# Kernel optimization log

Hardware: AMD Instinct MI355X
Metric: run time of the kernel (lower is better)

The kernel has to match this reference:

```python
import jax, jax.numpy as jnp
import numpy as np

B, S, DIM = 2, 2048, 1024
EXPERT_DIM = 256
N_S, N_R, TOP_K = 2, 32, 4
EPS = 1e-6


def setup_inputs() -> dict:
    key = jax.random.key(0)
    ks = jax.random.split(key, 12)
    s1 = 1.0 / np.sqrt(DIM)        # fan-in init scale for Linear(dim, expert_dim)
    s2 = 1.0 / np.sqrt(EXPERT_DIM)  # fan-in init scale for Linear(expert_dim, dim)
    return {
        "x": jax.random.normal(ks[0], (B, S, DIM), jnp.float32),
        "rms_w": jnp.ones((DIM,), jnp.float32),
        "centroids": jax.random.normal(ks[1], (N_R, DIM), jnp.float32),
        # shared experts, stacked along leading expert axis
        "sW1": jax.random.normal(ks[2], (N_S, DIM, EXPERT_DIM), jnp.float32) * s1,
        "sb1": jax.random.normal(ks[3], (N_S, EXPERT_DIM), jnp.float32) * s1,
        "sW2": jax.random.normal(ks[4], (N_S, EXPERT_DIM, DIM), jnp.float32) * s2,
        "sb2": jax.random.normal(ks[5], (N_S, DIM), jnp.float32) * s2,
        # routed experts
        "rW1": jax.random.normal(ks[6], (N_R, DIM, EXPERT_DIM), jnp.float32) * s1,
        "rb1": jax.random.normal(ks[7], (N_R, EXPERT_DIM), jnp.float32) * s1,
        "rW2": jax.random.normal(ks[8], (N_R, EXPERT_DIM, DIM), jnp.float32) * s2,
        "rb2": jax.random.normal(ks[9], (N_R, DIM), jnp.float32) * s2,
    }


def _rmsnorm(x, w):
    xf = x.astype(jnp.float32)
    n = xf * jax.lax.rsqrt(jnp.mean(xf * xf, axis=-1, keepdims=True) + EPS)
    return w * n.astype(x.dtype)


def _experts(xf, W1, b1, W2, b2):
    # xf: [T, D]; W1: [E, D, H]; returns [E, T, D]
    # Expert = Sequential(Linear, Linear, GELU) -> gelu applied AFTER second linear
    h = jnp.einsum('td,edh->eth', xf, W1) + b1[:, None, :]
    o = jnp.einsum('eth,ehd->etd', h, W2) + b2[:, None, :]
    return jax.nn.gelu(o, approximate=False)


def reference(x, rms_w, centroids, sW1, sb1, sW2, sb2, rW1, rb1, rW2, rb2):
    xn = _rmsnorm(x, rms_w)                      # [B, S, D]
    xf = xn.reshape(-1, DIM)                     # [T, D]
    T = xf.shape[0]

    # shared experts: summed dense output
    shared = _experts(xf, sW1, sb1, sW2, sb2).sum(axis=0)   # [T, D]

    # routing
    affinity = jax.nn.softmax(xf @ centroids.T, axis=-1)    # [T, E]
    topk_scores, topk_idx = jax.lax.top_k(affinity, TOP_K)
    mask = jnp.zeros_like(affinity).at[jnp.arange(T)[:, None], topk_idx].set(topk_scores)

    # dense-compute-then-mask, faithful to original module
    routed_all = _experts(xf, rW1, rb1, rW2, rb2)           # [E, T, D]
    routed = jnp.einsum('te,etd->td', mask, routed_all)     # [T, D]

    y = xn + (shared + routed).reshape(B, S, DIM)
    return y, affinity
```

## Files before the change

kernel.cpp:

```cpp
#include <hip/hip_runtime.h>
#include <hip/hip_bf16.h>
#include <math.h>

#define T_TOK 4096
#define DIM   1024
#define HDIM  256
#define N_SH  2
#define N_RT  32
#define N_E   34
#define TOPK  4
#define TB    128
#define MAXPB 200
#define NSLOT 6
#define OSW   34

typedef short bf16x8 __attribute__((ext_vector_type(8)));
typedef float f32x4  __attribute__((ext_vector_type(4)));
typedef unsigned short u16x8 __attribute__((ext_vector_type(8)));

__device__ __forceinline__ ushort f2b(float v) {
    __hip_bfloat16 h = __float2bfloat16(v);
    return *reinterpret_cast<const ushort*>(&h);
}
__device__ __forceinline__ float b2f(ushort u) {
    unsigned int x = ((unsigned int)u) << 16;
    return __uint_as_float(x);
}
__device__ __forceinline__ float gelu_tanh(float x) {
    float z = 0.7978845608028654f * (x + 0.044715f * x * x * x);
    float e = __expf(2.0f * z);
    float t = 1.0f - 2.0f / (e + 1.0f);
    return 0.5f * x * (1.0f + t);
}

__device__ __forceinline__ void gload_lds16(const ushort* g, ushort* l) {
    __builtin_amdgcn_global_load_lds(
        (const __attribute__((address_space(1))) void*)g,
        (__attribute__((address_space(3))) void*)l,
        16, 0, 0);
}

template<int K, int N>
__global__ __launch_bounds__(256) void pack_weights(
    const float* __restrict__ srcS, const float* __restrict__ srcR,
    ushort* __restrict__ dst)
{
    const int e = blockIdx.y;
    const float* src = (e < N_SH) ? (srcS + (size_t)e * K * N)
                                  : (srcR + (size_t)(e - N_SH) * K * N);
    const int kt  = K / 32;
    const int k32 = blockIdx.x % kt;
    const int nc  = blockIdx.x / kt;
    const int tid = threadIdx.x;

    __shared__ ushort ls[32][137];

    #pragma unroll
    for (int it = 0; it < 4; ++it) {
        const int row = it * 8 + (tid >> 5);
        const int c4  = tid & 31;
        const float4 v = *(const float4*)(src + (size_t)(k32 * 32 + row) * N
                                          + nc * 128 + c4 * 4);
        ls[row][c4 * 4 + 0] = f2b(v.x);
        ls[row][c4 * 4 + 1] = f2b(v.y);
        ls[row][c4 * 4 + 2] = f2b(v.z);
        ls[row][c4 * 4 + 3] = f2b(v.w);
    }
    __syncthreads();

    #pragma unroll
    for (int it = 0; it < 2; ++it) {
        const int t8   = tid >> 5;
        const int lane = it * 32 + (tid & 31);
        const int l16 = lane & 15, lk = lane >> 4;
        u16x8 o;
        #pragma unroll
        for (int j = 0; j < 8; ++j)
            o[j] = ls[lk * 8 + j][t8 * 16 + l16];
        const size_t tile = (size_t)(nc * 8 + t8) * kt + k32;
        *(u16x8*)(dst + (size_t)e * K * N + tile * 512 + lane * 8) = o;
    }
}

__global__ __launch_bounds__(256) void rms_router_kernel(
    const float* __restrict__ x, const float* __restrict__ rms_w,
    const float* __restrict__ cent,
    ushort* __restrict__ xnb, float* __restrict__ aff_out,
    int* __restrict__ tk_e, float* __restrict__ sscore)
{
    const int t0  = blockIdx.x * 4;
    const int tid = threadIdx.x;
    const int wid = tid >> 6;
    const int lane = tid & 63;
    const int t = t0 + wid;

    __shared__ float xsh[4][DIM];
    __shared__ float logits[4][N_RT];

    float4 xv[4], wv[4];
    float ss = 0.f;
    #pragma unroll
    for (int q = 0; q < 4; ++q) {
        xv[q] = ((const float4*)(x + (size_t)t * DIM))[lane + 64 * q];
        ss += xv[q].x*xv[q].x + xv[q].y*xv[q].y + xv[q].z*xv[q].z + xv[q].w*xv[q].w;
    }
    #pragma unroll
    for (int o = 32; o > 0; o >>= 1) ss += __shfl_down(ss, o);
    const float rstd = rsqrtf(__shfl(ss, 0) * (1.0f / (float)DIM) + 1e-6f);

    #pragma unroll
    for (int q = 0; q < 4; ++q)
        wv[q] = ((const float4*)rms_w)[lane + 64 * q];

    #pragma unroll
    for (int q = 0; q < 4; ++q) {
        float4 nv;
        nv.x = xv[q].x * rstd * wv[q].x;
        nv.y = xv[q].y * rstd * wv[q].y;
        nv.z = xv[q].z * rstd * wv[q].z;
        nv.w = xv[q].w * rstd * wv[q].w;
        ushort4 xb = make_ushort4(f2b(nv.x), f2b(nv.y), f2b(nv.z), f2b(nv.w));
        ((ushort4*)(xnb + (size_t)t * DIM))[lane + 64 * q] = xb;
        ((float4*)xsh[wid])[lane + 64 * q] = nv;
    }
    __syncthreads();

    #pragma unroll
    for (int ei = 0; ei < 8; ++ei) {
        const int e = wid * 8 + ei;
        const float4* c4 = (const float4*)(cent + (size_t)e * DIM);
        float a0 = 0.f, a1 = 0.f, a2 = 0.f, a3 = 0.f;
        #pragma unroll
        for (int q = 0; q < 4; ++q) {
            const float4 cv = c4[lane + 64 * q];
            const float4 x0 = ((const float4*)xsh[0])[lane + 64 * q];
            const float4 x1 = ((const float4*)xsh[1])[lane + 64 * q];
            const float4 x2 = ((const float4*)xsh[2])[lane + 64 * q];
            const float4 x3 = ((const float4*)xsh[3])[lane + 64 * q];
            a0 += cv.x*x0.x + cv.y*x0.y + cv.z*x0.z + cv.w*x0.w;
            a1 += cv.x*x1.x + cv.y*x1.y + cv.z*x1.z + cv.w*x1.w;
            a2 += cv.x*x2.x + cv.y*x2.y + cv.z*x2.z + cv.w*x2.w;
            a3 += cv.x*x3.x + cv.y*x3.y + cv.z*x3.z + cv.w*x3.w;
        }
        #pragma unroll
        for (int o = 32; o > 0; o >>= 1) {
            a0 += __shfl_down(a0, o);
            a1 += __shfl_down(a1, o);
            a2 += __shfl_down(a2, o);
            a3 += __shfl_down(a3, o);
        }
        if (lane == 0) {
            logits[0][e] = a0; logits[1][e] = a1;
            logits[2][e] = a2; logits[3][e] = a3;
        }
    }
    __syncthreads();

    {
        float v = (lane < N_RT) ? logits[wid][lane] : -INFINITY;
        float m = v;
        #pragma unroll
        for (int o = 32; o > 0; o >>= 1) m = fmaxf(m, __shfl_xor(m, o));
        float p = (lane < N_RT) ? expf(v - m) : 0.f;
        float s = p;
        #pragma unroll
        for (int o = 32; o > 0; o >>= 1) s += __shfl_xor(s, o);
        const float a = p / s;
        if (lane < N_RT) aff_out[(size_t)t * N_RT + lane] = a;
        if (lane < N_SH) sscore[(size_t)t * NSLOT + lane] = 1.f;

        float vv = (lane < N_RT) ? a : -1.f;
        #pragma unroll
        for (int it = 0; it < TOPK; ++it) {
            float mx = vv;
            #pragma unroll
            for (int o = 32; o > 0; o >>= 1) mx = fmaxf(mx, __shfl_xor(mx, o));
            unsigned long long msk = __ballot(vv == mx);
            int sel = __ffsll((long long)msk) - 1;
            sel = (sel < 0) ? 0 : (sel & (N_RT - 1));
            if (lane == 0) {
                tk_e[(size_t)t * TOPK + it] = sel;
                sscore[(size_t)t * NSLOT + 2 + it] = mx;
            }
            if (lane == sel) vv = -1.f;
        }
    }
}

__global__ __launch_bounds__(64) void scatter_kernel(
    const int* __restrict__ tk_e, int* __restrict__ counts, int* __restrict__ lists)
{
    const int e    = blockIdx.x;
    const int lane = threadIdx.x;
    const unsigned long long lt = (1ull << lane) - 1ull;
    int base = 0;
    int* lst = lists + (size_t)e * T_TOK;
    for (int c = 0; c < T_TOK * TOPK; c += 256) {
        const int4 v = *(const int4*)(tk_e + c + lane * 4);
        const bool p0 = (v.x == e), p1 = (v.y == e), p2 = (v.z == e), p3 = (v.w == e);
        const unsigned long long m0 = __ballot(p0);
        const unsigned long long m1 = __ballot(p1);
        const unsigned long long m2 = __ballot(p2);
        const unsigned long long m3 = __ballot(p3);
        const int c0 = __popcll(m0), c1 = __popcll(m1), c2 = __popcll(m2);
        if (p0) lst[base + __popcll(m0 & lt)] = c + lane * 4 + 0;
        if (p1) lst[base + c0 + __popcll(m1 & lt)] = c + lane * 4 + 1;
        if (p2) lst[base + c0 + c1 + __popcll(m2 & lt)] = c + lane * 4 + 2;
        if (p3) lst[base + c0 + c1 + c2 + __popcll(m3 & lt)] = c + lane * 4 + 3;
        base += c0 + c1 + c2 + __popcll(m3);
    }
    if (lane == 0) counts[e] = base;
}

__global__ __launch_bounds__(256) void residual_init(
    const ushort* __restrict__ xnb, float* __restrict__ y)
{
    const int idx = blockIdx.x * 256 + threadIdx.x;
    const ushort4 xr = *(const ushort4*)(xnb + (size_t)idx * 4);
    float4 a;
    a.x = b2f(xr.x); a.y = b2f(xr.y); a.z = b2f(xr.z); a.w = b2f(xr.w);
    ((float4*)y)[idx] = a;
}

template<bool ATOMIC>
__global__ __launch_bounds__(512, 2) void moe_mfma(
    const ushort* __restrict__ xnb,
    const ushort* __restrict__ W1p, const ushort* __restrict__ W2p,
    const float* __restrict__ sb1, const float* __restrict__ sb2,
    const float* __restrict__ rb1, const float* __restrict__ rb2,
    const int* __restrict__ counts, const int* __restrict__ lists,
    const float* __restrict__ sscore,
    ushort* __restrict__ sbuf, float* __restrict__ y)
{
    const int bi  = blockIdx.x;
    const int tid = threadIdx.x;

    __shared__ int    toks[TB];
    __shared__ int    orow[TB];
    __shared__ float  tscs[TB];
    __shared__ ushort hlds[TB * HDIM];
    __shared__ ushort astage[2 * 4096];
    __shared__ ushort ostage[8 * 64 * OSW];

    int e_full;
    const float *b1, *b2;

    if (bi < 64) {
        e_full = bi >> 5;
        const int tile = bi & 31;
        if (tid < TB) {
            const int t = tile * TB + tid;
            toks[tid] = t;
            orow[tid] = ATOMIC ? t : t * NSLOT + e_full;
            tscs[tid] = 1.f;
        }
        b1 = sb1 + e_full * HDIM;  b2 = sb2 + e_full * DIM;
    } else {
        const int j = bi - 64;
        const int b = j & 7, pos = j >> 3;
        int e = -1, tile = 0, accum = 0;
        #pragma unroll
        for (int g = 0; g < 4; ++g) {
            const int eg = b + 8 * g;
            const int tg = (counts[eg] + TB - 1) / TB;
            if (e < 0 && pos < accum + tg) { e = eg; tile = pos - accum; }
            accum += tg;
        }
        if (e < 0) return;
        e_full = N_SH + e;
        const int cnt = counts[e];
        if (tid < TB) {
            const int idx = tile * TB + tid;
            if (idx < cnt) {
                const int lv = lists[(size_t)e * T_TOK + idx];
                const int t = (lv >> 2) & (T_TOK - 1);
                toks[tid] = t;
                orow[tid] = ATOMIC ? t : t * NSLOT + 2 + (lv & 3);
                tscs[tid] = ATOMIC ? sscore[(size_t)t * NSLOT + 2 + (lv & 3)] : 0.f;
            } else {
                toks[tid] = 0;
                orow[tid] = ATOMIC ? 0 : T_TOK * NSLOT;
                tscs[tid] = 0.f;
            }
        }
        b1 = rb1 + e * HDIM;  b2 = rb2 + e * DIM;
    }
    __syncthreads();

    const int w = tid >> 6, lane = tid & 63;
    const int l16 = lane & 15, lk = lane >> 4;
    const int mh = w >> 2;
    const int nq = w & 3;

    const ushort* W1e = W1p + (size_t)e_full * DIM * HDIM;
    const ushort* W2e = W2p + (size_t)e_full * HDIM * DIM;

    {
        const ushort* asrc = xnb + (size_t)toks[w * 16 + (lane >> 2)] * DIM
                             + (lane & 3) * 8;
        gload_lds16(asrc, astage + w * 512);

        const ushort* bbase[4];
        #pragma unroll
        for (int ni = 0; ni < 4; ++ni)
            bbase[ni] = W1e + (size_t)((nq * 4 + ni) * 32) * 512 + lane * 8;

        f32x4 acc[4][4];
        #pragma unroll
        for (int mi = 0; mi < 4; ++mi)
            #pragma unroll
            for (int ni = 0; ni < 4; ++ni) acc[mi][ni] = (f32x4){0.f,0.f,0.f,0.f};

        bf16x8 bc[4];
        #pragma unroll
        for (int ni = 0; ni < 4; ++ni) bc[ni] = *(const bf16x8*)bbase[ni];
        __syncthreads();

        #pragma unroll 2
        for (int k32 = 0; k32 < 32; ++k32) {
            const int cur = k32 & 1;
            bf16x8 bn[4];
            if (k32 < 31) {
                gload_lds16(asrc + (k32 + 1) * 32,
                            astage + (cur ^ 1) * 4096 + w * 512);
                #pragma unroll
                for (int ni = 0; ni < 4; ++ni)
                    bn[ni] = *(const bf16x8*)(bbase[ni] + (size_t)(k32 + 1) * 512);
            }
            bf16x8 a[4];
            #pragma unroll
            for (int mi = 0; mi < 4; ++mi) {
                const int tloc = mh * 64 + mi * 16 + l16;
                a[mi] = *(const bf16x8*)(astage + cur * 4096 + tloc * 32 + lk * 8);
            }
            #pragma unroll
            for (int ni = 0; ni < 4; ++ni)
                #pragma unroll
                for (int mi = 0; mi < 4; ++mi)
                    acc[mi][ni] = __builtin_amdgcn_mfma_f32_16x16x32_bf16(a[mi], bc[ni], acc[mi][ni], 0, 0, 0);
            if (k32 < 31) {
                #pragma unroll
                for (int ni = 0; ni < 4; ++ni) bc[ni] = bn[ni];
            }
            __syncthreads();
        }

        #pragma unroll
        for (int ni = 0; ni < 4; ++ni) {
            const int n = nq * 64 + ni * 16 + l16;
            const float bv = b1[n];
            #pragma unroll
            for (int mi = 0; mi < 4; ++mi) {
                #pragma unroll
                for (int r = 0; r < 4; ++r) {
                    const int m = mh * 64 + mi * 16 + lk * 4 + r;
                    const int byte = (m * (HDIM * 2) + n * 2) ^ ((m & 7) << 4);
                    *(ushort*)((char*)hlds + byte) = f2b(acc[mi][ni][r] + bv);
                }
            }
        }
    }
    __syncthreads();

    {
        for (int jc = 0; jc < 4; ++jc) {
            f32x4 acc2[4][4];
            #pragma unroll
            for (int mi = 0; mi < 4; ++mi)
                #pragma unroll
                for (int ni = 0; ni < 4; ++ni) acc2[mi][ni] = (f32x4){0.f,0.f,0.f,0.f};

            const ushort* b2base[4];
            #pragma unroll
            for (int ni = 0; ni < 4; ++ni)
                b2base[ni] = W2e + (size_t)((jc * 16 + nq * 4 + ni) * 8) * 512 + lane * 8;

            bf16x8 bc2[4];
            #pragma unroll
            for (int ni = 0; ni < 4; ++ni) bc2[ni] = *(const bf16x8*)b2base[ni];

            #pragma unroll
            for (int k32 = 0; k32 < 8; ++k32) {
                bf16x8 a2[4];
                #pragma unroll
                for (int mi = 0; mi < 4; ++mi) {
                    const int m = mh * 64 + mi * 16 + l16;
                    const int byte = (m * (HDIM * 2) + (k32 * 32 + lk * 8) * 2) ^ ((m & 7) << 4);
                    a2[mi] = *(const bf16x8*)((const char*)hlds + byte);
                }
                bf16x8 bn2[4];
                if (k32 < 7) {
                    #pragma unroll
                    for (int ni = 0; ni < 4; ++ni)
                        bn2[ni] = *(const bf16x8*)(b2base[ni] + (size_t)(k32 + 1) * 512);
                }
                #pragma unroll
                for (int ni = 0; ni < 4; ++ni)
                    #pragma unroll
                    for (int mi = 0; mi < 4; ++mi)
                        acc2[mi][ni] = __builtin_amdgcn_mfma_f32_16x16x32_bf16(a2[mi], bc2[ni], acc2[mi][ni], 0, 0, 0);
                if (k32 < 7) {
                    #pragma unroll
                    for (int ni = 0; ni < 4; ++ni) bc2[ni] = bn2[ni];
                }
            }

            if (ATOMIC) {
                #pragma unroll
                for (int ni = 0; ni < 4; ++ni) {
                    const int n = jc * 256 + nq * 64 + ni * 16 + l16;
                    const float bv = b2[n];
                    #pragma unroll
                    for (int mi = 0; mi < 4; ++mi)
                        #pragma unroll
                        for (int r = 0; r < 4; ++r) {
                            const int m = mi * 16 + lk * 4 + r;
                            const float val = gelu_tanh(acc2[mi][ni][r] + bv) * tscs[mh * 64 + m];
                            atomicAdd(&y[(size_t)orow[mh * 64 + m] * DIM + n], val);
                        }
                }
            } else {
                ushort* os = ostage + w * (64 * OSW);
                #pragma unroll
                for (int p = 0; p < 2; ++p) {
                    asm volatile("s_waitcnt lgkmcnt(0)" ::: "memory");
                    #pragma unroll
                    for (int q = 0; q < 2; ++q) {
                        const int ni = p * 2 + q;
                        const float bv = b2[jc * 256 + nq * 64 + ni * 16 + l16];
                        #pragma unroll
                        for (int mi = 0; mi < 4; ++mi)
                            #pragma unroll
                            for (int r = 0; r < 4; ++r) {
                                const int m = mi * 16 + lk * 4 + r;
                                os[m * OSW + q * 16 + l16] = f2b(acc2[mi][ni][r] + bv);
                            }
                    }
                    asm volatile("s_waitcnt lgkmcnt(0)" ::: "memory");
                    #pragma unroll
                    for (int rr = 0; rr < 4; ++rr) {
                        const int m  = rr * 16 + (lane >> 2);
                        const int nl = (lane & 3) * 8;
                        u16x8 vv = *(const u16x8*)(os + m * OSW + nl);
                        *(u16x8*)(sbuf + (size_t)orow[mh * 64 + m] * DIM
                                  + jc * 256 + nq * 64 + p * 32 + nl) = vv;
                    }
                }
            }
        }
    }
}

__global__ __launch_bounds__(256) void gather_kernel(
    const ushort* __restrict__ sbuf, const float* __restrict__ sscore,
    const ushort* __restrict__ xnb, float* __restrict__ y)
{
    const int idx = blockIdx.x * 256 + threadIdx.x;
    const int t = idx >> 8;
    const int d = (idx & 255) * 4;
    const ushort4 xr = *(const ushort4*)(xnb + (size_t)t * DIM + d);
    float4 a;
    a.x = b2f(xr.x); a.y = b2f(xr.y); a.z = b2f(xr.z); a.w = b2f(xr.w);
    #pragma unroll
    for (int s = 0; s < NSLOT; ++s) {
        const float sc = sscore[(size_t)t * NSLOT + s];
        const ushort4 u = *(const ushort4*)(sbuf + ((size_t)t * NSLOT + s) * DIM + d);
        a.x += gelu_tanh(b2f(u.x)) * sc;
        a.y += gelu_tanh(b2f(u.y)) * sc;
        a.z += gelu_tanh(b2f(u.z)) * sc;
        a.w += gelu_tanh(b2f(u.w)) * sc;
    }
    ((float4*)y)[idx] = a;
}

extern "C" void kernel_launch(void* const* d_in, const int* in_sizes, int n_in,
                              void* d_out, int out_size, void* d_ws, size_t ws_size,
                              hipStream_t stream) {
    const float* x      = (const float*)d_in[0];
    const float* rms_w  = (const float*)d_in[1];
    const float* cent   = (const float*)d_in[2];
    const float* sW1    = (const float*)d_in[3];
    const float* sb1    = (const float*)d_in[4];
    const float* sW2    = (const float*)d_in[5];
    const float* sb2    = (const float*)d_in[6];
    const float* rW1    = (const float*)d_in[7];
    const float* rb1    = (const float*)d_in[8];
    const float* rW2    = (const float*)d_in[9];
    const float* rb2    = (const float*)d_in[10];

    float* y_out   = (float*)d_out;
    float* aff_out = (float*)d_out + (size_t)T_TOK * DIM;

    char* p = (char*)d_ws;
    size_t off = 0;
    auto take = [&](size_t b) {
        char* r = p + off;
        off += (b + 255) & ~(size_t)255;
        return r;
    };
    ushort* xnb    = (ushort*)take((size_t)T_TOK * DIM * 2);
    ushort* W1p    = (ushort*)take((size_t)N_E * DIM * HDIM * 2);
    ushort* W2p    = (ushort*)take((size_t)N_E * HDIM * DIM * 2);
    int*    counts = (int*)take(N_RT * sizeof(int));
    int*    lists  = (int*)take((size_t)N_RT * T_TOK * 4);
    float*  sscore = (float*)take((size_t)T_TOK * NSLOT * 4);
    int*    tk_e   = (int*)take((size_t)T_TOK * TOPK * 4);
    ushort* sbuf   = (ushort*)take(((size_t)T_TOK * NSLOT + TB) * DIM * 2);
    const bool slot_ok = (off <= ws_size);

    pack_weights<DIM, HDIM><<<dim3(64, N_E), dim3(256), 0, stream>>>(sW1, rW1, W1p);
    pack_weights<HDIM, DIM><<<dim3(64, N_E), dim3(256), 0, stream>>>(sW2, rW2, W2p);

    rms_router_kernel<<<dim3(T_TOK / 4), dim3(256), 0, stream>>>(
        x, rms_w, cent, xnb, aff_out, tk_e, sscore);

    scatter_kernel<<<dim3(N_RT), dim3(64), 0, stream>>>(tk_e, counts, lists);

    const int grid = 64 + 8 * MAXPB;
    if (slot_ok) {
        moe_mfma<false><<<dim3(grid), dim3(512), 0, stream>>>(
            xnb, W1p, W2p, sb1, sb2, rb1, rb2, counts, lists,
            sscore, sbuf, y_out);
        gather_kernel<<<dim3((T_TOK * DIM / 4) / 256), dim3(256), 0, stream>>>(
            sbuf, sscore, xnb, y_out);
    } else {
        residual_init<<<dim3((T_TOK * DIM / 4) / 256), dim3(256), 0, stream>>>(
            xnb, y_out);
        moe_mfma<true><<<dim3(grid), dim3(512), 0, stream>>>(
            xnb, W1p, W2p, sb1, sb2, rb1, rb2, counts, lists,
            sscore, sbuf, y_out);
    }
}
```

Measured before the change: 142.8 us.

## Stage expert weight tiles through LDS, shared across wave halves

Both expert GEMMs now load W1/W2 k-slices cooperatively into a double-buffered LDS buffer (bstage) with async global-to-LDS copies. Previously each wave loaded its B fragments straight from global into registers, so the two M-halves of waves fetched identical weight data twice. The second GEMM's nested jc/k loops are flattened into a single 32-step pipelined loop with a barrier per step. This halves weight traffic and frees registers, at the cost of 32KB more LDS, extra LDS reads and more __syncthreads.

```diff
diff --git a/kernel.cpp b/kernel.cpp
--- a/kernel.cpp
+++ b/kernel.cpp
@@ -240,6 +240,7 @@
     __shared__ float  tscs[TB];
     __shared__ ushort hlds[TB * HDIM];
     __shared__ ushort astage[2 * 4096];
+    __shared__ ushort bstage[2 * 8192];
     __shared__ ushort ostage[8 * 64 * OSW];
 
     int e_full;
@@ -299,35 +300,34 @@
         const ushort* asrc = xnb + (size_t)toks[w * 16 + (lane >> 2)] * DIM
                              + (lane & 3) * 8;
         gload_lds16(asrc, astage + w * 512);
-
-        const ushort* bbase[4];
-        #pragma unroll
-        for (int ni = 0; ni < 4; ++ni)
-            bbase[ni] = W1e + (size_t)((nq * 4 + ni) * 32) * 512 + lane * 8;
+        #pragma unroll
+        for (int s2 = 0; s2 < 2; ++s2) {
+            const int q = w * 2 + s2;
+            gload_lds16(W1e + (size_t)(q * 32 + 0) * 512 + lane * 8,
+                        bstage + q * 512);
+        }
 
         f32x4 acc[4][4];
         #pragma unroll
         for (int mi = 0; mi < 4; ++mi)
             #pragma unroll
             for (int ni = 0; ni < 4; ++ni) acc[mi][ni] = (f32x4){0.f,0.f,0.f,0.f};
-
-        bf16x8 bc[4];
-        #pragma unroll
-        for (int ni = 0; ni < 4; ++ni) bc[ni] = *(const bf16x8*)bbase[ni];
         __syncthreads();
 
         #pragma unroll 2
         for (int k32 = 0; k32 < 32; ++k32) {
             const int cur = k32 & 1;
-            bf16x8 bn[4];
             if (k32 < 31) {
                 gload_lds16(asrc + (k32 + 1) * 32,
                             astage + (cur ^ 1) * 4096 + w * 512);
                 #pragma unroll
-                for (int ni = 0; ni < 4; ++ni)
-                    bn[ni] = *(const bf16x8*)(bbase[ni] + (size_t)(k32 + 1) * 512);
-            }
-            bf16x8 a[4];
+                for (int s2 = 0; s2 < 2; ++s2) {
+                    const int q = w * 2 + s2;
+                    gload_lds16(W1e + (size_t)(q * 32 + k32 + 1) * 512 + lane * 8,
+                                bstage + (cur ^ 1) * 8192 + q * 512);
+                }
+            }
+            bf16x8 a[4], bf[4];
             #pragma unroll
             for (int mi = 0; mi < 4; ++mi) {
                 const int tloc = mh * 64 + mi * 16 + l16;
@@ -335,14 +335,20 @@
             }
             #pragma unroll
             for (int ni = 0; ni < 4; ++ni)
+                bf[ni] = *(const bf16x8*)(bstage + cur * 8192 + (nq * 4 + ni) * 512 + lane * 8);
+            #pragma unroll
+            for (int ni = 0; ni < 4; ++ni)
                 #pragma unroll
                 for (int mi = 0; mi < 4; ++mi)
-                    acc[mi][ni] = __builtin_amdgcn_mfma_f32_16x16x32_bf16(a[mi], bc[ni], acc[mi][ni], 0, 0, 0);
-            if (k32 < 31) {
-                #pragma unroll
-                for (int ni = 0; ni < 4; ++ni) bc[ni] = bn[ni];
-            }
+                    acc[mi][ni] = __builtin_amdgcn_mfma_f32_16x16x32_bf16(a[mi], bf[ni], acc[mi][ni], 0, 0, 0);
             __syncthreads();
+        }
+
+        #pragma unroll
+        for (int s2 = 0; s2 < 2; ++s2) {
+            const int q = w * 2 + s2;
+            gload_lds16(W2e + (size_t)((0 * 16 + q) * 8 + 0) * 512 + lane * 8,
+                        bstage + q * 512);
         }
 
         #pragma unroll
@@ -363,90 +369,95 @@
     __syncthreads();
 
     {
-        for (int jc = 0; jc < 4; ++jc) {
-            f32x4 acc2[4][4];
-            #pragma unroll
-            for (int mi = 0; mi < 4; ++mi)
+        f32x4 acc2[4][4];
+        #pragma unroll
+        for (int mi = 0; mi < 4; ++mi)
+            #pragma unroll
+            for (int ni = 0; ni < 4; ++ni) acc2[mi][ni] = (f32x4){0.f,0.f,0.f,0.f};
+
+        #pragma unroll 2
+        for (int s = 0; s < 32; ++s) {
+            const int jc  = s >> 3;
+            const int k32 = s & 7;
+            const int cur = s & 1;
+
+            if (s < 31) {
+                const int s2 = s + 1;
+                const int jc2 = s2 >> 3, kk2 = s2 & 7;
                 #pragma unroll
-                for (int ni = 0; ni < 4; ++ni) acc2[mi][ni] = (f32x4){0.f,0.f,0.f,0.f};
-
-            const ushort* b2base[4];
+                for (int q2 = 0; q2 < 2; ++q2) {
+                    const int q = w * 2 + q2;
+                    gload_lds16(W2e + (size_t)((jc2 * 16 + q) * 8 + kk2) * 512 + lane * 8,
+                                bstage + (cur ^ 1) * 8192 + q * 512);
+                }
+            }
+
+            bf16x8 a2[4], bf2[4];
+            #pragma unroll
+            for (int mi = 0; mi < 4; ++mi) {
+                const int m = mh * 64 + mi * 16 + l16;
+                const int byte = (m * (HDIM * 2) + (k32 * 32 + lk * 8) * 2) ^ ((m & 7) << 4);
+                a2[mi] = *(const bf16x8*)((const char*)hlds + byte);
+            }
             #pragma unroll
             for (int ni = 0; ni < 4; ++ni)
-                b2base[ni] = W2e + (size_t)((jc * 16 + nq * 4 + ni) * 8) * 512 + lane * 8;
-
-            bf16x8 bc2[4];
-            #pragma unroll
-            for (int ni = 0; ni < 4; ++ni) bc2[ni] = *(const bf16x8*)b2base[ni];
-
-            #pragma unroll
-            for (int k32 = 0; k32 < 8; ++k32) {
-                bf16x8 a2[4];
+                bf2[ni] = *(const bf16x8*)(bstage + cur * 8192 + (nq * 4 + ni) * 512 + lane * 8);
+
+            #pragma unroll
+            for (int ni = 0; ni < 4; ++ni)
                 #pragma unroll
-                for (int mi = 0; mi < 4; ++mi) {
-                    const int m = mh * 64 + mi * 16 + l16;
-                    const int byte = (m * (HDIM * 2) + (k32 * 32 + lk * 8) * 2) ^ ((m & 7) << 4);
-                    a2[mi] = *(const bf16x8*)((const char*)hlds + byte);
-                }
-                bf16x8 bn2[4];
-                if (k32 < 7) {
+                for (int mi = 0; mi < 4; ++mi)
+                    acc2[mi][ni] = __builtin_amdgcn_mfma_f32_16x16x32_bf16(a2[mi], bf2[ni], acc2[mi][ni], 0, 0, 0);
+
+            if (k32 == 7) {
+                if (ATOMIC) {
                     #pragma unroll
-                    for (int ni = 0; ni < 4; ++ni)
-                        bn2[ni] = *(const bf16x8*)(b2base[ni] + (size_t)(k32 + 1) * 512);
-                }
-                #pragma unroll
-                for (int ni = 0; ni < 4; ++ni)
-                    #pragma unroll
-                    for (int mi = 0; mi < 4; ++mi)
-                        acc2[mi][ni] = __builtin_amdgcn_mfma_f32_16x16x32_bf16(a2[mi], bc2[ni], acc2[mi][ni], 0, 0, 0);
-                if (k32 < 7) {
-                    #pragma unroll
-                    for (int ni = 0; ni < 4; ++ni) bc2[ni] = bn2[ni];
-                }
-            }
-
-            if (ATOMIC) {
-                #pragma unroll
-                for (int ni = 0; ni < 4; ++ni) {
-                    const int n = jc * 256 + nq * 64 + ni * 16 + l16;
-                    const float bv = b2[n];
-                    #pragma unroll
-                    for (int mi = 0; mi < 4; ++mi)
-                        #pragma unroll
-                        for (int r = 0; r < 4; ++r) {
-                            const int m = mi * 16 + lk * 4 + r;
-                            const float val = gelu_tanh(acc2[mi][ni][r] + bv) * tscs[mh * 64 + m];
-                            atomicAdd(&y[(size_t)orow[mh * 64 + m] * DIM + n], val);
-                        }
-                }
-            } else {
-                ushort* os = ostage + w * (64 * OSW);
-                #pragma unroll
-                for (int p = 0; p < 2; ++p) {
-                    asm volatile("s_waitcnt lgkmcnt(0)" ::: "memory");
-                    #pragma unroll
-                    for (int q = 0; q < 2; ++q) {
-                        const int ni = p * 2 + q;
-                        const float bv = b2[jc * 256 + nq * 64 + ni * 16 + l16];
+                    for (int ni = 0; ni < 4; ++ni) {
+                        const int n = jc * 256 + nq * 64 + ni * 16 + l16;
+                        const float bv = b2[n];
                         #pragma unroll
                         for (int mi = 0; mi < 4; ++mi)
                             #pragma unroll
                             for (int r = 0; r < 4; ++r) {
                                 const int m = mi * 16 + lk * 4 + r;
-                                os[m * OSW + q * 16 + l16] = f2b(acc2[mi][ni][r] + bv);
+                                const float val = gelu_tanh(acc2[mi][ni][r] + bv) * tscs[mh * 64 + m];
+                                atomicAdd(&y[(size_t)orow[mh * 64 + m] * DIM + n], val);
                             }
                     }
-                    asm volatile("s_waitcnt lgkmcnt(0)" ::: "memory");
+                } else {
+                    ushort* os = ostage + w * (64 * OSW);
                     #pragma unroll
-                    for (int rr = 0; rr < 4; ++rr) {
-                        const int m  = rr * 16 + (lane >> 2);
-                        const int nl = (lane & 3) * 8;
-                        u16x8 vv = *(const u16x8*)(os + m * OSW + nl);
-                        *(u16x8*)(sbuf + (size_t)orow[mh * 64 + m] * DIM
-                                  + jc * 256 + nq * 64 + p * 32 + nl) = vv;
+                    for (int p = 0; p < 2; ++p) {
+                        asm volatile("s_waitcnt lgkmcnt(0)" ::: "memory");
+                        #pragma unroll
+                        for (int q = 0; q < 2; ++q) {
+                            const int ni = p * 2 + q;
+                            const float bv = b2[jc * 256 + nq * 64 + ni * 16 + l16];
+                            #pragma unroll
+                            for (int mi = 0; mi < 4; ++mi)
+                                #pragma unroll
+                                for (int r = 0; r < 4; ++r) {
+                                    const int m = mi * 16 + lk * 4 + r;
+                                    os[m * OSW + q * 16 + l16] = f2b(acc2[mi][ni][r] + bv);
+                                }
+                        }
+                        asm volatile("s_waitcnt lgkmcnt(0)" ::: "memory");
+                        #pragma unroll
+                        for (int rr = 0; rr < 4; ++rr) {
+                            const int m  = rr * 16 + (lane >> 2);
+                            const int nl = (lane & 3) * 8;
+                            u16x8 vv = *(const u16x8*)(os + m * OSW + nl);
+                            *(u16x8*)(sbuf + (size_t)orow[mh * 64 + m] * DIM
+                                      + jc * 256 + nq * 64 + p * 32 + nl) = vv;
+                        }
                     }
                 }
-            }
+                #pragma unroll
+                for (int mi = 0; mi < 4; ++mi)
+                    #pragma unroll
+                    for (int ni = 0; ni < 4; ++ni) acc2[mi][ni] = (f32x4){0.f,0.f,0.f,0.f};
+            }
+            __syncthreads();
         }
     }
 }
```

After: 154.6 us. +8.3%, slower.

## Triple-buffer A staging in first GEMM with manual waitcnt and barriers

Applied to the files above, without the earlier changes.

Expands the LDS staging buffer for token activations from double to triple buffering so the A tile is prefetched two k-steps ahead via global_load_lds. The full __syncthreads is replaced with explicit vmcnt/lgkmcnt waits, raw s_barrier and sched_barrier fences, so waits cover only the loads actually needed. The goal is to hide global load latency in the first expert GEMM. It costs an extra 8 KB of LDS, which may reduce occupancy, and the hand-counted vmcnt values are fragile if the compiler reorders or adds loads.

```diff
diff --git a/kernel.cpp b/kernel.cpp
--- a/kernel.cpp
+++ b/kernel.cpp
@@ -39,6 +39,8 @@
         (__attribute__((address_space(3))) void*)l,
         16, 0, 0);
 }
+
+#define SBAR() __builtin_amdgcn_sched_barrier(0)
 
 template<int K, int N>
 __global__ __launch_bounds__(256) void pack_weights(
@@ -239,7 +241,7 @@
     __shared__ int    orow[TB];
     __shared__ float  tscs[TB];
     __shared__ ushort hlds[TB * HDIM];
-    __shared__ ushort astage[2 * 4096];
+    __shared__ ushort astage[3 * 4096];
     __shared__ ushort ostage[8 * 64 * OSW];
 
     int e_full;
@@ -298,7 +300,10 @@
     {
         const ushort* asrc = xnb + (size_t)toks[w * 16 + (lane >> 2)] * DIM
                              + (lane & 3) * 8;
-        gload_lds16(asrc, astage + w * 512);
+        SBAR();
+        gload_lds16(asrc,      astage + 0 * 4096 + w * 512);
+        gload_lds16(asrc + 32, astage + 1 * 4096 + w * 512);
+        SBAR();
 
         const ushort* bbase[4];
         #pragma unroll
@@ -314,25 +319,25 @@
         bf16x8 bc[4];
         #pragma unroll
         for (int ni = 0; ni < 4; ++ni) bc[ni] = *(const bf16x8*)bbase[ni];
-        __syncthreads();
+
+        asm volatile("s_waitcnt vmcnt(5)" ::: "memory");
+        __builtin_amdgcn_s_barrier();
+        SBAR();
 
         #pragma unroll 2
         for (int k32 = 0; k32 < 32; ++k32) {
-            const int cur = k32 & 1;
-            bf16x8 bn[4];
-            if (k32 < 31) {
-                gload_lds16(asrc + (k32 + 1) * 32,
-                            astage + (cur ^ 1) * 4096 + w * 512);
-                #pragma unroll
-                for (int ni = 0; ni < 4; ++ni)
-                    bn[ni] = *(const bf16x8*)(bbase[ni] + (size_t)(k32 + 1) * 512);
-            }
-            bf16x8 a[4];
+            const int cur = k32 % 3;
+            bf16x8 a[4], bn[4];
             #pragma unroll
             for (int mi = 0; mi < 4; ++mi) {
                 const int tloc = mh * 64 + mi * 16 + l16;
                 a[mi] = *(const bf16x8*)(astage + cur * 4096 + tloc * 32 + lk * 8);
             }
+            if (k32 < 31) {
+                #pragma unroll
+                for (int ni = 0; ni < 4; ++ni)
+                    bn[ni] = *(const bf16x8*)(bbase[ni] + (size_t)(k32 + 1) * 512);
+            }
             #pragma unroll
             for (int ni = 0; ni < 4; ++ni)
                 #pragma unroll
@@ -342,7 +347,21 @@
                 #pragma unroll
                 for (int ni = 0; ni < 4; ++ni) bc[ni] = bn[ni];
             }
-            __syncthreads();
+
+            if (k32 < 30) {
+                asm volatile("s_waitcnt lgkmcnt(0)" ::: "memory");
+                SBAR();
+                gload_lds16(asrc + (k32 + 2) * 32,
+                            astage + ((k32 + 2) % 3) * 4096 + w * 512);
+                SBAR();
+                asm volatile("s_waitcnt vmcnt(5)" ::: "memory");
+                __builtin_amdgcn_s_barrier();
+                SBAR();
+            } else if (k32 == 30) {
+                asm volatile("s_waitcnt vmcnt(4)" ::: "memory");
+                __builtin_amdgcn_s_barrier();
+                SBAR();
+            }
         }
 
         #pragma unroll
```

New measurement: 140.0 us. 2.0% less time.
